# Performance work log

Hardware: AMD Instinct MI355X
Metric: run time of the kernel (lower is better)

The kernel has to match this reference:

```python
import jax, jax.numpy as jnp
import numpy as np

B, NF, N, D, S, H = 16, 16, 1024, 128, 8, 128
EPS = 1e-8
SCALE = D ** -0.5


def _ln(x, g, b):
    m = x.mean(-1, keepdims=True)
    v = ((x - m) ** 2).mean(-1, keepdims=True)
    return (x - m) / jnp.sqrt(v + 1e-5) * g + b


def setup_inputs() -> dict:
    key = jax.random.key(0)
    ks = jax.random.split(key, 16)
    w = lambda k, *s: jax.random.normal(k, s, jnp.float32) * 0.02
    return {
        'inputs': jax.random.normal(ks[0], (B, NF, N, D), jnp.float32),
        'slots_init': jax.random.normal(ks[1], (1, S, D), jnp.float32),
        'Wq': w(ks[2], D, D), 'bq': jnp.zeros((D,), jnp.float32),
        'Wk': w(ks[3], D, D), 'bk': jnp.zeros((D,), jnp.float32),
        'Wv': w(ks[4], D, D), 'bv': jnp.zeros((D,), jnp.float32),
        'W1': w(ks[5], H, D), 'b1': jnp.zeros((H,), jnp.float32),
        'W2': w(ks[6], D, H), 'b2': jnp.zeros((D,), jnp.float32),
        'Wih': w(ks[7], 3 * D, D), 'Whh': w(ks[8], 3 * D, D),
        'bih': jnp.zeros((3 * D,), jnp.float32), 'bhh': jnp.zeros((3 * D,), jnp.float32),
        'g_in': jnp.ones((D,), jnp.float32), 'be_in': jnp.zeros((D,), jnp.float32),
        'g_sl': jnp.ones((D,), jnp.float32), 'be_sl': jnp.zeros((D,), jnp.float32),
        'g_ff': jnp.ones((D,), jnp.float32), 'be_ff': jnp.zeros((D,), jnp.float32),
    }


def reference(inputs, slots_init, Wq, bq, Wk, bk, Wv, bv, W1, b1, W2, b2,
              Wih, Whh, bih, bhh, g_in, be_in, g_sl, be_sl, g_ff, be_ff):
    def gru(x, h):  # PyTorch GRUCell, x/h: [BS, D]
        gi = x @ Wih.T + bih
        gh = h @ Whh.T + bhh
        r = jax.nn.sigmoid(gi[:, :D] + gh[:, :D])
        z = jax.nn.sigmoid(gi[:, D:2 * D] + gh[:, D:2 * D])
        n = jnp.tanh(gi[:, 2 * D:] + r * gh[:, 2 * D:])
        return (1.0 - z) * n + z * h

    def get_attention(slots, x):  # slots [B,S,D], x [B,N,D]
        slots_prev = slots
        xn = _ln(x, g_in, be_in)
        k = xn @ Wk.T + bk
        v = xn @ Wv.T + bv
        q = _ln(slots, g_sl, be_sl) @ Wq.T + bq
        dots = jnp.einsum('bid,bjd->bij', q, k) * SCALE  # [B,S,N]
        attn_ori = jax.nn.softmax(dots, axis=1) + EPS    # softmax over slots
        attn = attn_ori / attn_ori.sum(axis=-1, keepdims=True)
        updates = jnp.einsum('bjd,bij->bid', v, attn)    # [B,S,D]
        slots = gru(updates.reshape(-1, D), slots_prev.reshape(-1, D)).reshape(slots.shape[0], -1, D)
        ff = jax.nn.relu(_ln(slots, g_ff, be_ff) @ W1.T + b1) @ W2.T + b2
        return slots + ff, attn_ori

    slots = jnp.broadcast_to(slots_init, (inputs.shape[0], S, D))
    slots, _ = get_attention(slots, inputs[:, 0])  # warm-up on frame 0

    def body(carry, x_f):
        s, a = get_attention(carry, x_f)
        return s, (s, a)

    _, (slots_seq, attn_seq) = jax.lax.scan(body, slots, jnp.moveaxis(inputs, 1, 0))
    slots_out = jnp.moveaxis(slots_seq, 0, 1)  # [B,NF,S,D]
    attns = jnp.moveaxis(attn_seq, 0, 1)       # [B,NF,S,N]
    return slots_out, attns
```

## Files before the change

kernel.cpp:

```cpp
#include <hip/hip_runtime.h>

#define B_ 16
#define NF_ 16
#define N_ 1024
#define D_ 128
#define S_ 8
#define SCALE_ 0.08838834764831845f
#define NB 256
#define NT 512

struct SmemA {
  float Xt[64 * 129];
  float qWs[1024];
  float at[512];
  float rowsum[64], rowsum2[64];
  float qbs[8];
};
struct SmemB {
  float Pk[128], upd[128], hn[128], buf[128], hid[128], qsh[128], nrm[128];
  float gi[384], gh[384];
  float red[4], ssm;
};
union Smem { SmemA a; SmemB b; };

__device__ __forceinline__ float gload(const float* p) {
  return __hip_atomic_load(p, __ATOMIC_RELAXED, __HIP_MEMORY_SCOPE_AGENT);
}
__device__ __forceinline__ void gstore(float* p, float v) {
  __hip_atomic_store(p, v, __ATOMIC_RELAXED, __HIP_MEMORY_SCOPE_AGENT);
}

__device__ __forceinline__ void arrive(unsigned* c) {
  __syncthreads();
  if (threadIdx.x == 0) {
    __builtin_amdgcn_s_waitcnt(0);
    __hip_atomic_fetch_add(c, 1u, __ATOMIC_RELAXED, __HIP_MEMORY_SCOPE_AGENT);
  }
}
__device__ __forceinline__ void wait_for(unsigned* c, unsigned target) {
  if (threadIdx.x == 0) {
    while (__hip_atomic_load(c, __ATOMIC_RELAXED, __HIP_MEMORY_SCOPE_AGENT) < target)
      __builtin_amdgcn_s_sleep(1);
  }
  __syncthreads();
}

__device__ __forceinline__ float dot128f(const float* __restrict__ wrow, const float* x, float acc) {
  const float4* w = (const float4*)wrow;
#pragma unroll
  for (int i = 0; i < 32; ++i) {
    float4 v = w[i];
    const float4 xv = *(const float4*)(x + i * 4);
    acc += v.x * xv.x + v.y * xv.y + v.z * xv.z + v.w * xv.w;
  }
  return acc;
}

__device__ __forceinline__ void stats128(float v, int t, float* red, float& m, float& inv, float eps) {
  __syncthreads();
  float s = (t < 128) ? v : 0.f;
  float s2 = (t < 128) ? v * v : 0.f;
#pragma unroll
  for (int off = 32; off; off >>= 1) { s += __shfl_down(s, off); s2 += __shfl_down(s2, off); }
  if (t == 0)  { red[0] = s; red[2] = s2; }
  if (t == 64) { red[1] = s; red[3] = s2; }
  __syncthreads();
  m = (red[0] + red[1]) * (1.f / 128.f);
  float var = (red[2] + red[3]) * (1.f / 128.f) - m * m;
  inv = rsqrtf(var + eps);
}

__device__ __forceinline__ float sigm(float x) { return 1.f / (1.f + __expf(-x)); }
__device__ __forceinline__ float tanh_f(float x) { return 1.f - 2.f / (1.f + __expf(2.f * x)); }

__device__ void q_project(SmemB& B, const float* slot,
    const float* __restrict__ g_sl, const float* __restrict__ be_sl,
    const float* __restrict__ Wq, const float* __restrict__ bq,
    const float* __restrict__ Wk, const float* __restrict__ bk,
    float* qW_g, float* qb_g, int bs) {
  int t = threadIdx.x;
  float m, inv;
  float sv = (t < 128) ? slot[t] : 0.f;
  stats128(sv, t, B.red, m, inv, 1e-5f);
  if (t < 128) B.nrm[t] = (sv - m) * inv * g_sl[t] + be_sl[t];
  __syncthreads();
  if (t < 128) B.qsh[t] = dot128f(Wq + t * 128, B.nrm, bq[t]);
  __syncthreads();
  if (t < 128) {
    float a = 0.f;
#pragma unroll 16
    for (int d = 0; d < 128; ++d) a += B.qsh[d] * Wk[d * 128 + t];
    gstore(&qW_g[bs * 128 + t], a);
    float p = B.qsh[t] * bk[t];
#pragma unroll
    for (int off = 32; off; off >>= 1) p += __shfl_down(p, off);
    if (t == 0)  B.red[0] = p;
    if (t == 64) B.red[1] = p;
  }
  __syncthreads();
  if (t == 0) gstore(&qb_g[bs], B.red[0] + B.red[1]);
}

__global__ __launch_bounds__(NT) void slot_persist(
    const float* __restrict__ x, const float* __restrict__ slots_init,
    const float* __restrict__ Wq, const float* __restrict__ bq,
    const float* __restrict__ Wk, const float* __restrict__ bk,
    const float* __restrict__ Wv, const float* __restrict__ bv,
    const float* __restrict__ W1, const float* __restrict__ b1,
    const float* __restrict__ W2, const float* __restrict__ b2,
    const float* __restrict__ Wih, const float* __restrict__ Whh,
    const float* __restrict__ bih, const float* __restrict__ bhh,
    const float* __restrict__ g_in, const float* __restrict__ be_in,
    const float* __restrict__ g_sl, const float* __restrict__ be_sl,
    const float* __restrict__ g_ff, const float* __restrict__ be_ff,
    float* out_slots, float* out_attn,
    unsigned* cntA, unsigned* cntB,
    float* qW_g, float* qb_g, float* P_part, float* S_part) {
  __shared__ __align__(16) Smem sm;
  __shared__ __align__(16) float slot_sh[128];
  __shared__ float gs[128], bs_[128];
  int t = threadIdx.x, bid = blockIdx.x;
  int b = bid >> 4, jt = bid & 15;
  bool isB = (jt < 8);
  unsigned* cA = cntA + (b << 6);
  unsigned* cB = cntB + (b << 6);

  if (t < 128) { gs[t] = g_in[t]; bs_[t] = be_in[t]; }
  if (isB) {
    if (t < 128) slot_sh[t] = slots_init[jt * 128 + t];
    q_project(sm.b, slot_sh, g_sl, be_sl, Wq, bq, Wk, bk, qW_g, qb_g, b * 8 + jt);
    arrive(cB);
  }
  float4 pf[4];
  {
    const float* xsrc = x + (((long)b * NF_ + 0) * N_ + jt * 64) * D_;
#pragma unroll
    for (int i = 0; i < 4; ++i) {
      int ch = t + i * 512;
      pf[i] = *(const float4*)(xsrc + (ch >> 5) * 128 + (ch & 31) * 4);
    }
  }
  wait_for(cB, 8u);

  for (int it = 0; it < 17; ++it) {
    int f = (it == 0) ? 0 : it - 1;
    int wo = it > 0;
#pragma unroll
    for (int i = 0; i < 4; ++i) {
      int ch = t + i * 512;
      float* dst = sm.a.Xt + (ch >> 5) * 129 + (ch & 31) * 4;
      dst[0] = pf[i].x; dst[1] = pf[i].y; dst[2] = pf[i].z; dst[3] = pf[i].w;
    }
    sm.a.qWs[t] = gload(&qW_g[b * 1024 + t]);
    sm.a.qWs[512 + t] = gload(&qW_g[b * 1024 + 512 + t]);
    if (t < 8) sm.a.qbs[t] = gload(&qb_g[b * 8 + t]);
    __syncthreads();
    int r8 = t >> 3, p8 = t & 7;
    {
      const float* row = sm.a.Xt + r8 * 129 + p8 * 16;
      float s1 = 0.f, s2 = 0.f;
#pragma unroll
      for (int i = 0; i < 16; ++i) { float v = row[i]; s1 += v; s2 += v * v; }
      s1 += __shfl_down(s1, 1); s2 += __shfl_down(s2, 1);
      s1 += __shfl_down(s1, 2); s2 += __shfl_down(s2, 2);
      s1 += __shfl_down(s1, 4); s2 += __shfl_down(s2, 4);
      if (p8 == 0) { sm.a.rowsum[r8] = s1; sm.a.rowsum2[r8] = s2; }
    }
    __syncthreads();
    {
      float m = sm.a.rowsum[r8] * (1.f / 128.f);
      float var = sm.a.rowsum2[r8] * (1.f / 128.f) - m * m;
      float inv = rsqrtf(var + 1e-5f);
      float* row = sm.a.Xt + r8 * 129 + p8 * 16;
      const float* gg = gs + p8 * 16;
      const float* bb = bs_ + p8 * 16;
#pragma unroll
      for (int i = 0; i < 16; ++i) row[i] = (row[i] - m) * inv * gg[i] + bb[i];
    }
    __syncthreads();
    {
      int s = t >> 6, j = t & 63;
      const float* qq = sm.a.qWs + s * 128;
      const float* xr = sm.a.Xt + j * 129;
      float d = 0.f;
#pragma unroll
      for (int k = 0; k < 128; ++k) d += xr[k] * qq[k];
      sm.a.at[s * 64 + j] = (d + sm.a.qbs[s]) * SCALE_;
    }
    __syncthreads();
    if (t < 64) {
      float vals[8], mx = -1e30f;
#pragma unroll
      for (int s = 0; s < 8; ++s) { vals[s] = sm.a.at[s * 64 + t]; mx = fmaxf(mx, vals[s]); }
      float sum = 0.f;
#pragma unroll
      for (int s = 0; s < 8; ++s) { vals[s] = __expf(vals[s] - mx); sum += vals[s]; }
      float rr = 1.f / sum;
#pragma unroll
      for (int s = 0; s < 8; ++s) { vals[s] = vals[s] * rr + 1e-8f; sm.a.at[s * 64 + t] = vals[s]; }
      if (wo) {
#pragma unroll
        for (int s = 0; s < 8; ++s)
          out_attn[(((long)b * NF_ + f) * S_ + s) * N_ + jt * 64 + t] = vals[s];
      }
    }
    __syncthreads();
    {
      int w = t >> 6, lane = t & 63;
      float v = sm.a.at[w * 64 + lane];
#pragma unroll
      for (int off = 32; off; off >>= 1) v += __shfl_down(v, off);
      if (lane == 0) gstore(&S_part[(b * 16 + jt) * 8 + w], v);
    }
    {
      int k2 = t & 127, h = t >> 7;
      float u0 = 0.f, u1 = 0.f;
      const float* a0 = sm.a.at + h * 64;
      const float* a1 = sm.a.at + (h + 4) * 64;
#pragma unroll 8
      for (int j = 0; j < 64; ++j) {
        float xv = sm.a.Xt[j * 129 + k2];
        u0 += xv * a0[j]; u1 += xv * a1[j];
      }
      float* pp = P_part + (long)(b * 16 + jt) * 8 * 128;
      gstore(&pp[h * 128 + k2], u0);
      gstore(&pp[(h + 4) * 128 + k2], u1);
    }
    arrive(cA);
    if (it < 16) {
      const float* xsrc = x + (((long)b * NF_ + it) * N_ + jt * 64) * D_;
#pragma unroll
      for (int i = 0; i < 4; ++i) {
        int ch = t + i * 512;
        pf[i] = *(const float4*)(xsrc + (ch >> 5) * 128 + (ch & 31) * 4);
      }
    }
    if (isB) {
      wait_for(cA, 16u * (it + 1));
      SmemB& B = sm.b;
      int s = jt;
      if (t < 128) {
        float pa = 0.f;
#pragma unroll
        for (int j = 0; j < 16; ++j)
          pa += gload(&P_part[(long)((b * 16 + j) * 8 + s) * 128 + t]);
        B.Pk[t] = pa;
      }
      if (t < 16) {
        float sv = gload(&S_part[(b * 16 + t) * 8 + s]);
        sv += __shfl_down(sv, 8); sv += __shfl_down(sv, 4);
        sv += __shfl_down(sv, 2); sv += __shfl_down(sv, 1);
        if (t == 0) B.ssm = sv;
      }
      __syncthreads();
      if (t < 128) {
        float a = dot128f(Wv + t * 128, B.Pk, 0.f);
        B.upd[t] = a / B.ssm + bv[t];
      } else {
        int r = t - 128;
        B.gh[r] = dot128f(Whh + r * 128, slot_sh, bhh[r]);
      }
      __syncthreads();
      if (t < 384) B.gi[t] = dot128f(Wih + t * 128, B.upd, bih[t]);
      __syncthreads();
      if (t < 128) {
        float r = sigm(B.gi[t] + B.gh[t]);
        float z = sigm(B.gi[128 + t] + B.gh[128 + t]);
        float n = tanh_f(B.gi[256 + t] + r * B.gh[256 + t]);
        B.hn[t] = (1.f - z) * n + z * slot_sh[t];
      }
      float m, inv;
      float hv = (t < 128) ? B.hn[t] : 0.f;
      stats128(hv, t, B.red, m, inv, 1e-5f);
      if (t < 128) B.buf[t] = (hv - m) * inv * g_ff[t] + be_ff[t];
      __syncthreads();
      if (t < 128) B.hid[t] = fmaxf(dot128f(W1 + t * 128, B.buf, b1[t]), 0.f);
      __syncthreads();
      if (t < 128) {
        float ffv = dot128f(W2 + t * 128, B.hid, b2[t]);
        float sn = B.hn[t] + ffv;
        slot_sh[t] = sn;
        if (wo) out_slots[(((long)b * NF_ + f) * S_ + s) * D_ + t] = sn;
      }
      __syncthreads();
      if (it < 16) {
        q_project(B, slot_sh, g_sl, be_sl, Wq, bq, Wk, bk, qW_g, qb_g, b * 8 + s);
        arrive(cB);
        wait_for(cB, 8u * (it + 2));
      }
    } else {
      if (it < 16) wait_for(cB, 8u * (it + 2));
    }
  }
}

extern "C" void kernel_launch(void* const* d_in, const int* in_sizes, int n_in,
                              void* d_out, int out_size, void* d_ws, size_t ws_size,
                              hipStream_t stream) {
  const float* inputs     = (const float*)d_in[0];
  const float* slots_init = (const float*)d_in[1];
  const float* Wq  = (const float*)d_in[2];
  const float* bq  = (const float*)d_in[3];
  const float* Wk  = (const float*)d_in[4];
  const float* bk  = (const float*)d_in[5];
  const float* Wv  = (const float*)d_in[6];
  const float* bv  = (const float*)d_in[7];
  const float* W1  = (const float*)d_in[8];
  const float* b1  = (const float*)d_in[9];
  const float* W2  = (const float*)d_in[10];
  const float* b2  = (const float*)d_in[11];
  const float* Wih = (const float*)d_in[12];
  const float* Whh = (const float*)d_in[13];
  const float* bih = (const float*)d_in[14];
  const float* bhh = (const float*)d_in[15];
  const float* g_in  = (const float*)d_in[16];
  const float* be_in = (const float*)d_in[17];
  const float* g_sl  = (const float*)d_in[18];
  const float* be_sl = (const float*)d_in[19];
  const float* g_ff  = (const float*)d_in[20];
  const float* be_ff = (const float*)d_in[21];

  float* out_slots = (float*)d_out;
  float* out_attn  = out_slots + (size_t)B_ * NF_ * S_ * D_;

  char* ws = (char*)d_ws;
  unsigned* cntA = (unsigned*)ws;
  unsigned* cntB = (unsigned*)(ws + 4096);
  float* qW_g    = (float*)(ws + 16384);
  float* qb_g    = (float*)(ws + 16384 + 65536);
  float* P_part  = (float*)(ws + 16384 + 66048);
  float* S_part  = (float*)(ws + 16384 + 66048 + 1048576);

  hipMemsetAsync(d_ws, 0, 16384, stream);

  slot_persist<<<NB, NT, 0, stream>>>(inputs, slots_init, Wq, bq, Wk, bk, Wv, bv,
      W1, b1, W2, b2, Wih, Whh, bih, bhh, g_in, be_in, g_sl, be_sl, g_ff, be_ff,
      out_slots, out_attn, cntA, cntB, qW_g, qb_g, P_part, S_part);
}
```

Measured before the change: 775.8 us.

## Fold Wq·Wk and Wih·Wv into precomputed weights, vectorize shared-memory loops

Adds a precompute kernel that multiplies Wih by Wv and Wq by Wk, along with their folded biases. The serial slot-update path then needs fewer dependent matvecs: the query-key projection becomes a single matvec, and the update goes straight into the GRU input gates, with the division by the attention sum applied afterwards. Separately, the Xt tile is padded to a row stride of 132 so the LayerNorm, dot-product and update loops can use float4 shared-memory accesses. The cost is an extra kernel launch per call and a change in floating-point rounding order.

Result: faster. 716.9 us (-7.6%).

```diff
diff --git a/kernel.cpp b/kernel.cpp
--- a/kernel.cpp
+++ b/kernel.cpp
@@ -10,16 +10,19 @@
 #define NT 512
 
 struct SmemA {
-  float Xt[64 * 129];
+  float Xt[64 * 132];
   float qWs[1024];
   float at[512];
   float rowsum[64], rowsum2[64];
   float qbs[8];
 };
 struct SmemB {
-  float Pk[128], upd[128], hn[128], buf[128], hid[128], qsh[128], nrm[128];
-  float gi[384], gh[384];
-  float red[4], ssm;
+  float Pk[128];
+  float gh[384];
+  float gi[384];
+  float hn[128], buf[128], hid[128], nrm[128];
+  float red[8];
+  float ssm;
 };
 union Smem { SmemA a; SmemB b; };
 
@@ -67,58 +70,100 @@
   __syncthreads();
   m = (red[0] + red[1]) * (1.f / 128.f);
   float var = (red[2] + red[3]) * (1.f / 128.f) - m * m;
-  inv = rsqrtf(var + eps);
+  inv = rsqrtf(var + 1e-5f);
 }
 
 __device__ __forceinline__ float sigm(float x) { return 1.f / (1.f + __expf(-x)); }
 __device__ __forceinline__ float tanh_f(float x) { return 1.f - 2.f / (1.f + __expf(2.f * x)); }
 
-__device__ void q_project(SmemB& B, const float* slot,
+__device__ void q_project(SmemB& Bm, const float* slot,
     const float* __restrict__ g_sl, const float* __restrict__ be_sl,
-    const float* __restrict__ Wq, const float* __restrict__ bq,
-    const float* __restrict__ Wk, const float* __restrict__ bk,
+    const float* __restrict__ Wqk, const float* __restrict__ bqk,
+    const float* __restrict__ wqbk, const float* __restrict__ bqbk,
     float* qW_g, float* qb_g, int bs) {
   int t = threadIdx.x;
   float m, inv;
   float sv = (t < 128) ? slot[t] : 0.f;
-  stats128(sv, t, B.red, m, inv, 1e-5f);
-  if (t < 128) B.nrm[t] = (sv - m) * inv * g_sl[t] + be_sl[t];
-  __syncthreads();
-  if (t < 128) B.qsh[t] = dot128f(Wq + t * 128, B.nrm, bq[t]);
+  stats128(sv, t, Bm.red, m, inv, 1e-5f);
+  if (t < 128) Bm.nrm[t] = (sv - m) * inv * g_sl[t] + be_sl[t];
   __syncthreads();
   if (t < 128) {
-    float a = 0.f;
-#pragma unroll 16
-    for (int d = 0; d < 128; ++d) a += B.qsh[d] * Wk[d * 128 + t];
+    float a = dot128f(Wqk + t * 128, Bm.nrm, bqk[t]);
     gstore(&qW_g[bs * 128 + t], a);
-    float p = B.qsh[t] * bk[t];
+    float p = wqbk[t] * Bm.nrm[t];
 #pragma unroll
     for (int off = 32; off; off >>= 1) p += __shfl_down(p, off);
-    if (t == 0)  B.red[0] = p;
-    if (t == 64) B.red[1] = p;
-  }
-  __syncthreads();
-  if (t == 0) gstore(&qb_g[bs], B.red[0] + B.red[1]);
+    if (t == 0)  Bm.red[4] = p;
+    if (t == 64) Bm.red[5] = p;
+  }
+  __syncthreads();
+  if (t == 0) gstore(&qb_g[bs], Bm.red[4] + Bm.red[5] + bqbk[0]);
+}
+
+__global__ __launch_bounds__(128) void precomp(
+    const float* __restrict__ Wih, const float* __restrict__ bih,
+    const float* __restrict__ Wv, const float* __restrict__ bv,
+    const float* __restrict__ Wq, const float* __restrict__ bq,
+    const float* __restrict__ Wk, const float* __restrict__ bk,
+    float* Wiv, float* bihv, float* Wqk, float* bqk, float* wqbk, float* bqbk) {
+  __shared__ float r2[2];
+  int r = blockIdx.x, t = threadIdx.x;
+  if (r < 384) {
+    float acc = 0.f;
+#pragma unroll 8
+    for (int k = 0; k < 128; ++k) acc += Wih[r * 128 + k] * Wv[k * 128 + t];
+    Wiv[r * 128 + t] = acc;
+    float p = Wih[r * 128 + t] * bv[t];
+#pragma unroll
+    for (int off = 32; off; off >>= 1) p += __shfl_down(p, off);
+    if ((t & 63) == 0) r2[t >> 6] = p;
+    __syncthreads();
+    if (t == 0) bihv[r] = r2[0] + r2[1] + bih[r];
+  } else {
+    int c = r - 384;
+    float acc = 0.f;
+#pragma unroll 8
+    for (int dd = 0; dd < 128; ++dd) acc += Wk[dd * 128 + c] * Wq[dd * 128 + t];
+    Wqk[c * 128 + t] = acc;
+    float p = Wk[t * 128 + c] * bq[t];
+#pragma unroll
+    for (int off = 32; off; off >>= 1) p += __shfl_down(p, off);
+    if ((t & 63) == 0) r2[t >> 6] = p;
+    __syncthreads();
+    if (t == 0) bqk[c] = r2[0] + r2[1];
+    if (c == 0) {
+      float a2 = 0.f;
+#pragma unroll 8
+      for (int dd = 0; dd < 128; ++dd) a2 += Wq[dd * 128 + t] * bk[dd];
+      wqbk[t] = a2;
+      float p2 = bq[t] * bk[t];
+#pragma unroll
+      for (int off = 32; off; off >>= 1) p2 += __shfl_down(p2, off);
+      __syncthreads();
+      if ((t & 63) == 0) r2[t >> 6] = p2;
+      __syncthreads();
+      if (t == 0) bqbk[0] = r2[0] + r2[1];
+    }
+  }
 }
 
 __global__ __launch_bounds__(NT) void slot_persist(
     const float* __restrict__ x, const float* __restrict__ slots_init,
-    const float* __restrict__ Wq, const float* __restrict__ bq,
-    const float* __restrict__ Wk, const float* __restrict__ bk,
-    const float* __restrict__ Wv, const float* __restrict__ bv,
+    const float* __restrict__ Whh, const float* __restrict__ bhh,
     const float* __restrict__ W1, const float* __restrict__ b1,
     const float* __restrict__ W2, const float* __restrict__ b2,
-    const float* __restrict__ Wih, const float* __restrict__ Whh,
-    const float* __restrict__ bih, const float* __restrict__ bhh,
     const float* __restrict__ g_in, const float* __restrict__ be_in,
     const float* __restrict__ g_sl, const float* __restrict__ be_sl,
     const float* __restrict__ g_ff, const float* __restrict__ be_ff,
+    const float* __restrict__ Wiv, const float* __restrict__ bihv,
+    const float* __restrict__ Wqk, const float* __restrict__ bqk,
+    const float* __restrict__ wqbk, const float* __restrict__ bqbk,
     float* out_slots, float* out_attn,
     unsigned* cntA, unsigned* cntB,
     float* qW_g, float* qb_g, float* P_part, float* S_part) {
   __shared__ __align__(16) Smem sm;
   __shared__ __align__(16) float slot_sh[128];
-  __shared__ float gs[128], bs_[128];
+  __shared__ __align__(16) float gs[128], bs_[128];
   int t = threadIdx.x, bid = blockIdx.x;
   int b = bid >> 4, jt = bid & 15;
   bool isB = (jt < 8);
@@ -128,7 +173,7 @@
   if (t < 128) { gs[t] = g_in[t]; bs_[t] = be_in[t]; }
   if (isB) {
     if (t < 128) slot_sh[t] = slots_init[jt * 128 + t];
-    q_project(sm.b, slot_sh, g_sl, be_sl, Wq, bq, Wk, bk, qW_g, qb_g, b * 8 + jt);
+    q_project(sm.b, slot_sh, g_sl, be_sl, Wqk, bqk, wqbk, bqbk, qW_g, qb_g, b * 8 + jt);
     arrive(cB);
   }
   float4 pf[4];
@@ -148,8 +193,7 @@
 #pragma unroll
     for (int i = 0; i < 4; ++i) {
       int ch = t + i * 512;
-      float* dst = sm.a.Xt + (ch >> 5) * 129 + (ch & 31) * 4;
-      dst[0] = pf[i].x; dst[1] = pf[i].y; dst[2] = pf[i].z; dst[3] = pf[i].w;
+      *(float4*)&sm.a.Xt[(ch >> 5) * 132 + (ch & 31) * 4] = pf[i];
     }
     sm.a.qWs[t] = gload(&qW_g[b * 1024 + t]);
     sm.a.qWs[512 + t] = gload(&qW_g[b * 1024 + 512 + t]);
@@ -157,10 +201,14 @@
     __syncthreads();
     int r8 = t >> 3, p8 = t & 7;
     {
-      const float* row = sm.a.Xt + r8 * 129 + p8 * 16;
+      const float4* row4 = (const float4*)(sm.a.Xt + r8 * 132 + p8 * 16);
       float s1 = 0.f, s2 = 0.f;
 #pragma unroll
-      for (int i = 0; i < 16; ++i) { float v = row[i]; s1 += v; s2 += v * v; }
+      for (int i = 0; i < 4; ++i) {
+        float4 v = row4[i];
+        s1 += v.x + v.y + v.z + v.w;
+        s2 += v.x * v.x + v.y * v.y + v.z * v.z + v.w * v.w;
+      }
       s1 += __shfl_down(s1, 1); s2 += __shfl_down(s2, 1);
       s1 += __shfl_down(s1, 2); s2 += __shfl_down(s2, 2);
       s1 += __shfl_down(s1, 4); s2 += __shfl_down(s2, 4);
@@ -171,20 +219,30 @@
       float m = sm.a.rowsum[r8] * (1.f / 128.f);
       float var = sm.a.rowsum2[r8] * (1.f / 128.f) - m * m;
       float inv = rsqrtf(var + 1e-5f);
-      float* row = sm.a.Xt + r8 * 129 + p8 * 16;
-      const float* gg = gs + p8 * 16;
-      const float* bb = bs_ + p8 * 16;
-#pragma unroll
-      for (int i = 0; i < 16; ++i) row[i] = (row[i] - m) * inv * gg[i] + bb[i];
+      float4* row4 = (float4*)(sm.a.Xt + r8 * 132 + p8 * 16);
+      const float4* gg4 = (const float4*)(gs + p8 * 16);
+      const float4* bb4 = (const float4*)(bs_ + p8 * 16);
+#pragma unroll
+      for (int i = 0; i < 4; ++i) {
+        float4 v = row4[i], g4 = gg4[i], b4 = bb4[i];
+        v.x = (v.x - m) * inv * g4.x + b4.x;
+        v.y = (v.y - m) * inv * g4.y + b4.y;
+        v.z = (v.z - m) * inv * g4.z + b4.z;
+        v.w = (v.w - m) * inv * g4.w + b4.w;
+        row4[i] = v;
+      }
     }
     __syncthreads();
     {
       int s = t >> 6, j = t & 63;
-      const float* qq = sm.a.qWs + s * 128;
-      const float* xr = sm.a.Xt + j * 129;
+      const float4* qq4 = (const float4*)(sm.a.qWs + s * 128);
+      const float4* xr4 = (const float4*)(sm.a.Xt + j * 132);
       float d = 0.f;
 #pragma unroll
-      for (int k = 0; k < 128; ++k) d += xr[k] * qq[k];
+      for (int k = 0; k < 32; ++k) {
+        float4 xv = xr4[k], qv = qq4[k];
+        d += xv.x * qv.x + xv.y * qv.y + xv.z * qv.z + xv.w * qv.w;
+      }
       sm.a.at[s * 64 + j] = (d + sm.a.qbs[s]) * SCALE_;
     }
     __syncthreads();
@@ -217,10 +275,16 @@
       float u0 = 0.f, u1 = 0.f;
       const float* a0 = sm.a.at + h * 64;
       const float* a1 = sm.a.at + (h + 4) * 64;
-#pragma unroll 8
-      for (int j = 0; j < 64; ++j) {
-        float xv = sm.a.Xt[j * 129 + k2];
-        u0 += xv * a0[j]; u1 += xv * a1[j];
+#pragma unroll
+      for (int j0 = 0; j0 < 64; j0 += 4) {
+        float4 av0 = *(const float4*)(a0 + j0);
+        float4 av1 = *(const float4*)(a1 + j0);
+        float x0 = sm.a.Xt[(j0 + 0) * 132 + k2];
+        float x1 = sm.a.Xt[(j0 + 1) * 132 + k2];
+        float x2 = sm.a.Xt[(j0 + 2) * 132 + k2];
+        float x3 = sm.a.Xt[(j0 + 3) * 132 + k2];
+        u0 += av0.x * x0 + av0.y * x1 + av0.z * x2 + av0.w * x3;
+        u1 += av1.x * x0 + av1.y * x1 + av1.z * x2 + av1.w * x3;
       }
       float* pp = P_part + (long)(b * 16 + jt) * 8 * 128;
       gstore(&pp[h * 128 + k2], u0);
@@ -237,54 +301,52 @@
     }
     if (isB) {
       wait_for(cA, 16u * (it + 1));
-      SmemB& B = sm.b;
+      SmemB& Bm = sm.b;
       int s = jt;
       if (t < 128) {
         float pa = 0.f;
 #pragma unroll
         for (int j = 0; j < 16; ++j)
           pa += gload(&P_part[(long)((b * 16 + j) * 8 + s) * 128 + t]);
-        B.Pk[t] = pa;
-      }
-      if (t < 16) {
-        float sv = gload(&S_part[(b * 16 + t) * 8 + s]);
+        Bm.Pk[t] = pa;
+      } else {
+        int r = t - 128;
+        Bm.gh[r] = dot128f(Whh + r * 128, slot_sh, bhh[r]);
+      }
+      __syncthreads();
+      if (t < 384) {
+        Bm.gi[t] = dot128f(Wiv + (long)t * 128, Bm.Pk, 0.f);
+      } else if (t >= 448 && t < 464) {
+        int tl = t - 448;
+        float sv = gload(&S_part[(b * 16 + tl) * 8 + s]);
         sv += __shfl_down(sv, 8); sv += __shfl_down(sv, 4);
         sv += __shfl_down(sv, 2); sv += __shfl_down(sv, 1);
-        if (t == 0) B.ssm = sv;
+        if (tl == 0) Bm.ssm = sv;
       }
       __syncthreads();
       if (t < 128) {
-        float a = dot128f(Wv + t * 128, B.Pk, 0.f);
-        B.upd[t] = a / B.ssm + bv[t];
-      } else {
-        int r = t - 128;
-        B.gh[r] = dot128f(Whh + r * 128, slot_sh, bhh[r]);
-      }
-      __syncthreads();
-      if (t < 384) B.gi[t] = dot128f(Wih + t * 128, B.upd, bih[t]);
+        float invss = 1.f / Bm.ssm;
+        float gr = sigm(Bm.gi[t] * invss + bihv[t] + Bm.gh[t]);
+        float gz = sigm(Bm.gi[128 + t] * invss + bihv[128 + t] + Bm.gh[128 + t]);
+        float gn = tanh_f(Bm.gi[256 + t] * invss + bihv[256 + t] + gr * Bm.gh[256 + t]);
+        Bm.hn[t] = (1.f - gz) * gn + gz * slot_sh[t];
+      }
+      float m, inv;
+      float hv = (t < 128) ? Bm.hn[t] : 0.f;
+      stats128(hv, t, Bm.red, m, inv, 1e-5f);
+      if (t < 128) Bm.buf[t] = (hv - m) * inv * g_ff[t] + be_ff[t];
+      __syncthreads();
+      if (t < 128) Bm.hid[t] = fmaxf(dot128f(W1 + t * 128, Bm.buf, b1[t]), 0.f);
       __syncthreads();
       if (t < 128) {
-        float r = sigm(B.gi[t] + B.gh[t]);
-        float z = sigm(B.gi[128 + t] + B.gh[128 + t]);
-        float n = tanh_f(B.gi[256 + t] + r * B.gh[256 + t]);
-        B.hn[t] = (1.f - z) * n + z * slot_sh[t];
-      }
-      float m, inv;
-      float hv = (t < 128) ? B.hn[t] : 0.f;
-      stats128(hv, t, B.red, m, inv, 1e-5f);
-      if (t < 128) B.buf[t] = (hv - m) * inv * g_ff[t] + be_ff[t];
-      __syncthreads();
-      if (t < 128) B.hid[t] = fmaxf(dot128f(W1 + t * 128, B.buf, b1[t]), 0.f);
-      __syncthreads();
-      if (t < 128) {
-        float ffv = dot128f(W2 + t * 128, B.hid, b2[t]);
-        float sn = B.hn[t] + ffv;
+        float ffv = dot128f(W2 + t * 128, Bm.hid, b2[t]);
+        float sn = Bm.hn[t] + ffv;
         slot_sh[t] = sn;
         if (wo) out_slots[(((long)b * NF_ + f) * S_ + s) * D_ + t] = sn;
       }
       __syncthreads();
       if (it < 16) {
-        q_project(B, slot_sh, g_sl, be_sl, Wq, bq, Wk, bk, qW_g, qb_g, b * 8 + s);
+        q_project(Bm, slot_sh, g_sl, be_sl, Wqk, bqk, wqbk, bqbk, qW_g, qb_g, b * 8 + s);
         arrive(cB);
         wait_for(cB, 8u * (it + 2));
       }
@@ -326,14 +388,23 @@
   char* ws = (char*)d_ws;
   unsigned* cntA = (unsigned*)ws;
   unsigned* cntB = (unsigned*)(ws + 4096);
-  float* qW_g    = (float*)(ws + 16384);
-  float* qb_g    = (float*)(ws + 16384 + 65536);
-  float* P_part  = (float*)(ws + 16384 + 66048);
-  float* S_part  = (float*)(ws + 16384 + 66048 + 1048576);
+  float* Wiv   = (float*)(ws + 16384);
+  float* bihv  = (float*)(ws + 212992);
+  float* WqkW  = (float*)(ws + 214528);
+  float* bqk   = (float*)(ws + 280064);
+  float* wqbk  = (float*)(ws + 280576);
+  float* bqbk  = (float*)(ws + 281088);
+  float* qW_g  = (float*)(ws + 281344);
+  float* qb_g  = (float*)(ws + 346880);
+  float* P_part = (float*)(ws + 347392);
+  float* S_part = (float*)(ws + 1395968);
 
   hipMemsetAsync(d_ws, 0, 16384, stream);
 
-  slot_persist<<<NB, NT, 0, stream>>>(inputs, slots_init, Wq, bq, Wk, bk, Wv, bv,
-      W1, b1, W2, b2, Wih, Whh, bih, bhh, g_in, be_in, g_sl, be_sl, g_ff, be_ff,
+  precomp<<<512, 128, 0, stream>>>(Wih, bih, Wv, bv, Wq, bq, Wk, bk,
+                                   Wiv, bihv, WqkW, bqk, wqbk, bqbk);
+  slot_persist<<<NB, NT, 0, stream>>>(inputs, slots_init, Whh, bhh,
+      W1, b1, W2, b2, g_in, be_in, g_sl, be_sl, g_ff, be_ff,
+      Wiv, bihv, WqkW, bqk, wqbk, bqbk,
       out_slots, out_attn, cntA, cntB, qW_g, qb_g, P_part, S_part);
 }
```
